# Performance work log

Hardware: AMD Instinct MI355X
Metric: run time of the kernel (lower is better)

Reference implementation:

```python
import jax, jax.numpy as jnp
import numpy as np

DIM = 1024
N_HEADS = 16
HEAD_DIM = DIM // N_HEADS
SCALE = HEAD_DIM ** 0.5


def setup_inputs() -> dict:
    key = jax.random.key(0)
    k_x, k_wqkv, k_bqkv, k_wp, k_bp = jax.random.split(key, 5)
    B, S = 4, 2048
    x = jax.random.normal(k_x, (B, S, DIM), dtype=jnp.float32)
    # Linear params stored input-major: y = x @ W + b
    std_qkv = 1.0 / np.sqrt(DIM)
    W_qkv = jax.random.uniform(k_wqkv, (DIM, 3 * DIM), jnp.float32, -std_qkv, std_qkv)
    b_qkv = jax.random.uniform(k_bqkv, (3 * DIM,), jnp.float32, -std_qkv, std_qkv)
    W_proj = jax.random.uniform(k_wp, (DIM, DIM), jnp.float32, -std_qkv, std_qkv)
    b_proj = jax.random.uniform(k_bp, (DIM,), jnp.float32, -std_qkv, std_qkv)
    return {"x": x, "W_qkv": W_qkv, "b_qkv": b_qkv, "W_proj": W_proj, "b_proj": b_proj}


def reference(x, W_qkv, b_qkv, W_proj, b_proj):
    B, S, D = x.shape
    qkv = x @ W_qkv + b_qkv                       # [B,S,3D]
    Q, K, V = jnp.split(qkv, 3, axis=-1)          # each [B,S,D]
    def heads(t):                                 # [B,S,D] -> [B,H,S,hd]
        return t.reshape(B, S, N_HEADS, HEAD_DIM).transpose(0, 2, 1, 3)
    Q, K, V = heads(Q), heads(K), heads(V)
    scores = jnp.einsum('bhqd,bhkd->bhqk', Q, K) / SCALE   # [B,H,S,S]
    attn = jax.nn.softmax(scores, axis=-1)
    out = jnp.einsum('bhqk,bhkd->bhqd', attn, V)           # [B,H,S,hd]
    out = out.transpose(0, 2, 1, 3).reshape(B, S, D)
    return out @ W_proj + b_proj
```

## Files before the change

### kernel.cpp

```cpp
#include <hip/hip_runtime.h>
#include <hip/hip_bf16.h>

typedef __attribute__((ext_vector_type(8))) __bf16 bf16x8;
typedef __attribute__((ext_vector_type(4))) float f32x4;
typedef __attribute__((ext_vector_type(16))) float f32x16;
typedef __attribute__((ext_vector_type(4))) unsigned int u32x4;

#define DIM 1024
#define NHEADS 16
#define HDIM 64
#define BATCH 4
#define SEQ 2048
#define ROWS (BATCH * SEQ)
#define SCL 0.18033688011112042f

__device__ inline unsigned short f2bf(float f) {
    __hip_bfloat16 h = __float2bfloat16(f);
    return *reinterpret_cast<unsigned short*>(&h);
}

__device__ inline unsigned int packbf2(float a, float b) {
    unsigned short ua = __builtin_bit_cast(unsigned short, (__bf16)a);
    unsigned short ub = __builtin_bit_cast(unsigned short, (__bf16)b);
    return (unsigned int)ua | ((unsigned int)ub << 16);
}

typedef const __attribute__((address_space(1))) unsigned int* gas_ptr;
typedef __attribute__((address_space(3))) unsigned int* las_ptr;
__device__ inline void gload16(const void* g, void* l) {
    __builtin_amdgcn_global_load_lds((gas_ptr)g, (las_ptr)l, 16, 0, 0);
}

__global__ __launch_bounds__(256) void prologue(const float* __restrict__ x,
                                                unsigned short* __restrict__ x_bf,
                                                const float* __restrict__ W_qkv,
                                                unsigned short* __restrict__ WqkvT,
                                                const float* __restrict__ W_proj,
                                                unsigned short* __restrict__ WprojT) {
    __shared__ float tile[32][33];
    const int blk = blockIdx.x;
    if (blk < 8192) {
        int i = blk * 256 + threadIdx.x;
        float4 v = ((const float4*)x)[i];
        ushort4 o;
        o.x = f2bf(v.x); o.y = f2bf(v.y); o.z = f2bf(v.z); o.w = f2bf(v.w);
        ((ushort4*)x_bf)[i] = o;
        return;
    }
    const float* in; unsigned short* outp; int C, srows, bx, byy; float scl;
    if (blk < 11264) {
        int t = blk - 8192;
        in = W_qkv; outp = WqkvT; C = 3 * DIM; srows = DIM; scl = SCL;
        bx = t % 96; byy = t / 96;
    } else {
        int t = blk - 11264;
        in = W_proj; outp = WprojT; C = DIM; srows = 0; scl = 1.f;
        bx = t & 31; byy = t >> 5;
    }
    const int R = DIM;
    int c0 = bx * 32, r0 = byy * 32;
    int tx = threadIdx.x & 31, ty = threadIdx.x >> 5;
#pragma unroll
    for (int i = 0; i < 32; i += 8) {
        int r = r0 + ty + i, c = c0 + tx;
        tile[ty + i][tx] = in[(size_t)r * C + c];
    }
    __syncthreads();
#pragma unroll
    for (int i = 0; i < 32; i += 8) {
        int orow = c0 + ty + i, oc = r0 + tx;
        float v = tile[tx][ty + i];
        if (orow < srows) v *= scl;
        outp[(size_t)orow * R + oc] = f2bf(v);
    }
}

__global__ __launch_bounds__(256) void gemm_bt_bias(const unsigned short* __restrict__ A,
                                                    const unsigned short* __restrict__ Bt,
                                                    const float* __restrict__ bias,
                                                    unsigned short* __restrict__ Cq,
                                                    unsigned short* __restrict__ Kp,
                                                    unsigned short* __restrict__ Vp,
                                                    float* __restrict__ Cf,
                                                    int M, int N, int K, int qcols) {
    __shared__ unsigned short SMEM[18432];
    unsigned short* As0 = SMEM;
    unsigned short* Bs0 = SMEM + 8192;
    const int tid = threadIdx.x;
    const int lane = tid & 63, wave = tid >> 6;
    const int wm = (wave >> 1) * 64, wn = (wave & 1) * 64;
    const int nwg = gridDim.x * gridDim.y;
    const int gflat = blockIdx.y * gridDim.x + blockIdx.x;
    const int bidx = (gflat & 7) * (nwg >> 3) + (gflat >> 3);
    const int bx = bidx % gridDim.x, byy = bidx / gridDim.x;
    const int rowA = byy * 128, rowB = bx * 128;
    const int fr = lane & 15, fo = (lane >> 4) * 8;

    f32x4 acc[4][4] = {};

    for (int k0 = 0; k0 < K; k0 += 64) {
#pragma unroll
        for (int kc = 0; kc < 2; kc++) {
#pragma unroll
            for (int c = 0; c < 2; c++) {
                int o = c * 4096 + tid * 16;
                int r = o >> 6, cb = o & 63;
                int ldsb = c * 4096 + wave * 1024;
                gload16((const char*)A + ((size_t)(rowA + r) * K + k0 + kc * 32) * 2 + cb,
                        (char*)As0 + kc * 8192 + ldsb);
                gload16((const char*)Bt + ((size_t)(rowB + r) * K + k0 + kc * 32) * 2 + cb,
                        (char*)Bs0 + kc * 8192 + ldsb);
            }
        }
        __syncthreads();
#pragma unroll
        for (int kc = 0; kc < 2; kc++) {
            bf16x8 af[4], bfr[4];
#pragma unroll
            for (int i = 0; i < 4; i++) {
                af[i]  = *(const bf16x8*)(As0 + kc * 4096 + (wm + i * 16 + fr) * 32 + fo);
                bfr[i] = *(const bf16x8*)(Bs0 + kc * 4096 + (wn + i * 16 + fr) * 32 + fo);
            }
#pragma unroll
            for (int mi = 0; mi < 4; mi++)
#pragma unroll
                for (int ni = 0; ni < 4; ni++)
                    acc[mi][ni] = __builtin_amdgcn_mfma_f32_16x16x32_bf16(af[mi], bfr[ni],
                                                                          acc[mi][ni], 0, 0, 0);
        }
        __syncthreads();
    }

    const int cn = lane & 15, cm = (lane >> 4) * 4;
    const int gn0 = rowB + wn;

    if (Cf) {
        for (int ni = 0; ni < 4; ni++) {
            int gn = gn0 + ni * 16 + cn;
            float bv = bias[gn];
            if (gn < qcols) bv *= SCL;
            for (int mi = 0; mi < 4; mi++) {
#pragma unroll
                for (int r = 0; r < 4; r++) {
                    int gm = rowA + wm + mi * 16 + cm + r;
                    Cf[(size_t)gm * N + gn] = acc[mi][ni][r] + bv;
                }
            }
        }
    } else if (gn0 < 1024) {
        for (int ni = 0; ni < 4; ni++) {
            int gn = gn0 + ni * 16 + cn;
            float bv = bias[gn];
            if (gn < qcols) bv *= SCL;
            for (int mi = 0; mi < 4; mi++) {
#pragma unroll
                for (int r = 0; r < 4; r++) {
                    int gm = rowA + wm + mi * 16 + cm + r;
                    Cq[(size_t)gm * 1024 + gn] = f2bf(acc[mi][ni][r] + bv);
                }
            }
        }
    } else {
        unsigned short* Lw = SMEM + wave * (64 * 72);
        for (int ni = 0; ni < 4; ni++) {
            float bv = bias[gn0 + ni * 16 + cn];
            for (int mi = 0; mi < 4; mi++) {
#pragma unroll
                for (int r = 0; r < 4; r++)
                    Lw[(mi * 16 + cm + r) * 72 + ni * 16 + cn] = f2bf(acc[mi][ni][r] + bv);
            }
        }
        __builtin_amdgcn_s_waitcnt(0);
        const int b = rowA >> 11, s0g = rowA & 2047;
        const int mm = lane & 31, hh = lane >> 5;
        if (gn0 < 2048) {
            const int h = (gn0 - 1024) >> 6;
            const size_t by = (size_t)(b * 16 + h);
            const int kub = (s0g + wm) >> 5;
#pragma unroll
            for (int f = 0; f < 8; f++) {
                int ktl = f >> 2, ks = f & 3;
                uint4 d = *(const uint4*)&Lw[(ktl * 32 + mm) * 72 + ks * 16 + hh * 8];
                *(uint4*)(Kp + ((by * 64 + kub + ktl) * 4 + ks) * 512 + lane * 8) = d;
            }
        } else {
            const int h = (gn0 - 2048) >> 6;
            const size_t by = (size_t)(b * 16 + h);
            const int vub = (s0g + wm) >> 4;
#pragma unroll
            for (int f = 0; f < 8; f++) {
                int ksl = f >> 1, dt = f & 1;
                unsigned short tmp[8];
#pragma unroll
                for (int j = 0; j < 8; j++)
                    tmp[j] = Lw[(ksl * 16 + (j & 3) + 8 * (j >> 2) + 4 * hh) * 72 + dt * 32 + mm];
                *(uint4*)(Vp + ((by * 128 + vub + ksl) * 2 + dt) * 512 + lane * 8) =
                    *(uint4*)tmp;
            }
        }
    }
}

__device__ inline void softmax_pv(const f32x16& cfrag, const bf16x8 vf[2][2],
                                  f32x16& o0, f32x16& o1, float& psum) {
    unsigned int pk[8];
    float es[8];
#pragma unroll
    for (int p = 0; p < 8; p++) {
        float e0 = __builtin_amdgcn_exp2f(cfrag[2 * p]);
        float e1 = __builtin_amdgcn_exp2f(cfrag[2 * p + 1]);
        es[p] = e0 + e1;
        pk[p] = packbf2(e0, e1);
    }
    psum += ((es[0] + es[1]) + (es[2] + es[3])) + ((es[4] + es[5]) + (es[6] + es[7]));
    u32x4 lo = {pk[0], pk[1], pk[2], pk[3]};
    u32x4 hi = {pk[4], pk[5], pk[6], pk[7]};
    bf16x8 pa0 = __builtin_bit_cast(bf16x8, lo);
    bf16x8 pa1 = __builtin_bit_cast(bf16x8, hi);
    o0 = __builtin_amdgcn_mfma_f32_32x32x16_bf16(pa0, vf[0][0], o0, 0, 0, 0);
    o1 = __builtin_amdgcn_mfma_f32_32x32x16_bf16(pa0, vf[0][1], o1, 0, 0, 0);
    o0 = __builtin_amdgcn_mfma_f32_32x32x16_bf16(pa1, vf[1][0], o0, 0, 0, 0);
    o1 = __builtin_amdgcn_mfma_f32_32x32x16_bf16(pa1, vf[1][1], o1, 0, 0, 0);
}

__device__ inline void attn_step(const bf16x8 kf[4], const bf16x8 vf[2][2],
                                 const bf16x8 qf[2][4], f32x16 oacc[2][2], float psum[2]) {
    f32x16 cf0 = {}, cf1 = {};
#pragma unroll
    for (int ks = 0; ks < 4; ks++)
        cf0 = __builtin_amdgcn_mfma_f32_32x32x16_bf16(kf[ks], qf[0][ks], cf0, 0, 0, 0);
#pragma unroll
    for (int ks = 0; ks < 4; ks++)
        cf1 = __builtin_amdgcn_mfma_f32_32x32x16_bf16(kf[ks], qf[1][ks], cf1, 0, 0, 0);
    softmax_pv(cf0, vf, oacc[0][0], oacc[0][1], psum[0]);
    softmax_pv(cf1, vf, oacc[1][0], oacc[1][1], psum[1]);
}

__global__ __launch_bounds__(256, 2) void attn_kernel(const unsigned short* __restrict__ Qb,
                                                      const unsigned short* __restrict__ Kp,
                                                      const unsigned short* __restrict__ Vp,
                                                      unsigned short* __restrict__ attnb) {
    __shared__ float Po[2][8 * 256];
    __shared__ float Pl[2][128];
    const int tid = threadIdx.x;
    const int lane = tid & 63, wave = tid >> 6;
    const int qpair = wave >> 1, ksplit = wave & 1;
    const int m31 = lane & 31, h = lane >> 5;
    const int gflat = blockIdx.y * gridDim.x + blockIdx.x;
    const int xcd = gflat & 7, slot = gflat >> 3;
    const int by = xcd * 8 + (slot >> 4);
    const int qb = slot & 15;
    const int b = by >> 4;
    const int bS = b * SEQ, hcol = (by & 15) * HDIM;
    const int q0 = qb * 128 + qpair * 64;

    bf16x8 qf[2][4];
#pragma unroll
    for (int qt = 0; qt < 2; qt++)
#pragma unroll
        for (int ks = 0; ks < 4; ks++)
            qf[qt][ks] = *(const bf16x8*)(Qb + (size_t)(bS + q0 + qt * 32 + m31) * 1024 +
                                          hcol + ks * 16 + h * 8);

    f32x16 oacc[2][2] = {};
    float psum[2] = {0.f, 0.f};

    const unsigned short* kbase = Kp + (size_t)by * 64 * 2048 + lane * 8;
    const unsigned short* vbase = Vp + (size_t)by * 128 * 1024 + lane * 8;

    const int ku0 = ksplit * 32;
    bf16x8 kfa[4], kfb[4];
    {
        const unsigned short* kp = kbase + (size_t)ku0 * 2048;
#pragma unroll
        for (int ks = 0; ks < 4; ks++) kfa[ks] = *(const bf16x8*)(kp + ks * 512);
    }
    for (int ki = 0; ki < 32; ki += 2) {
        {
            int ku = ku0 + ki;
            bf16x8 vf[2][2];
#pragma unroll
            for (int ks = 0; ks < 2; ks++) {
                const unsigned short* vp = vbase + ((size_t)ku * 2 + ks) * 1024;
                vf[ks][0] = *(const bf16x8*)(vp);
                vf[ks][1] = *(const bf16x8*)(vp + 512);
            }
            const unsigned short* kpn = kbase + (size_t)(ku + 1) * 2048;
#pragma unroll
            for (int ks = 0; ks < 4; ks++) kfb[ks] = *(const bf16x8*)(kpn + ks * 512);
            attn_step(kfa, vf, qf, oacc, psum);
        }
        {
            int ku = ku0 + ki + 1;
            bf16x8 vf[2][2];
#pragma unroll
            for (int ks = 0; ks < 2; ks++) {
                const unsigned short* vp = vbase + ((size_t)ku * 2 + ks) * 1024;
                vf[ks][0] = *(const bf16x8*)(vp);
                vf[ks][1] = *(const bf16x8*)(vp + 512);
            }
            int kup = ku0 + ((ki + 2 < 32) ? (ki + 2) : 31);
            const unsigned short* kpn = kbase + (size_t)kup * 2048;
#pragma unroll
            for (int ks = 0; ks < 4; ks++) kfa[ks] = *(const bf16x8*)(kpn + ks * 512);
            attn_step(kfb, vf, qf, oacc, psum);
        }
    }

#pragma unroll
    for (int qt = 0; qt < 2; qt++) {
        if (ksplit == 1) {
#pragma unroll
            for (int dt = 0; dt < 2; dt++)
#pragma unroll
                for (int c = 0; c < 4; c++) {
                    f32x4 v = {oacc[qt][dt][c * 4 + 0], oacc[qt][dt][c * 4 + 1],
                               oacc[qt][dt][c * 4 + 2], oacc[qt][dt][c * 4 + 3]};
                    *(f32x4*)&Po[qpair][(dt * 4 + c) * 256 + lane * 4] = v;
                }
            if (qt == 0)
                *(float2*)&Pl[qpair][lane * 2] = make_float2(psum[0], psum[1]);
        }
        __syncthreads();
        if (ksplit == 0) {
#pragma unroll
            for (int dt = 0; dt < 2; dt++)
#pragma unroll
                for (int c = 0; c < 4; c++) {
                    f32x4 v = *(const f32x4*)&Po[qpair][(dt * 4 + c) * 256 + lane * 4];
#pragma unroll
                    for (int j = 0; j < 4; j++) oacc[qt][dt][c * 4 + j] += v[j];
                }
            if (qt == 0) {
                float2 pl = *(const float2*)&Pl[qpair][lane * 2];
                psum[0] += pl.x; psum[1] += pl.y;
            }
        }
        if (qt == 0) __syncthreads();
    }

    if (ksplit == 0) {
#pragma unroll
        for (int qt = 0; qt < 2; qt++) {
            float lt = psum[qt] + __shfl_xor(psum[qt], 32, 64);
            float rl = 1.f / lt;
#pragma unroll
            for (int r = 0; r < 16; r++) {
                int row = (r & 3) + 8 * (r >> 2) + 4 * h;
                float rlr = __shfl(rl, row, 64);
                size_t orow = (size_t)(bS + q0 + qt * 32 + row) * 1024 + hcol;
                attnb[orow + m31]      = f2bf(oacc[qt][0][r] * rlr);
                attnb[orow + 32 + m31] = f2bf(oacc[qt][1][r] * rlr);
            }
        }
    }
}

extern "C" void kernel_launch(void* const* d_in, const int* in_sizes, int n_in,
                              void* d_out, int out_size, void* d_ws, size_t ws_size,
                              hipStream_t stream) {
    const float* x      = (const float*)d_in[0];
    const float* W_qkv  = (const float*)d_in[1];
    const float* b_qkv  = (const float*)d_in[2];
    const float* W_proj = (const float*)d_in[3];
    const float* b_proj = (const float*)d_in[4];
    float* out = (float*)d_out;

    char* ws = (char*)d_ws;
    unsigned short* x_bf   = (unsigned short*)(ws);
    unsigned short* WqkvT  = (unsigned short*)(ws + 16777216);
    unsigned short* Qb     = (unsigned short*)(ws + 23068672);
    unsigned short* Kp     = (unsigned short*)(ws + 39845888);
    unsigned short* Vp     = (unsigned short*)(ws + 56623104);
    unsigned short* WprojT = (unsigned short*)(ws + 73400320);
    unsigned short* attnb  = (unsigned short*)(ws);

    prologue<<<12288, 256, 0, stream>>>(x, x_bf, W_qkv, WqkvT, W_proj, WprojT);

    gemm_bt_bias<<<dim3(3 * DIM / 128, ROWS / 128), 256, 0, stream>>>(
        x_bf, WqkvT, b_qkv, Qb, Kp, Vp, nullptr, ROWS, 3 * DIM, DIM, DIM);

    attn_kernel<<<dim3(SEQ / 128, BATCH * NHEADS), 256, 0, stream>>>(Qb, Kp, Vp, attnb);

    gemm_bt_bias<<<dim3(DIM / 128, ROWS / 128), 256, 0, stream>>>(
        attnb, WprojT, b_proj, nullptr, nullptr, nullptr, out, ROWS, DIM, DIM, 0);
}
```

Measured before the change: 261.8 us.

## Add dedicated 256x256-tile pipelined QKV GEMM with fused K/V packing

Replaces the generic 128x128 GEMM for the QKV projection with a dedicated 512-thread kernel using 256x256 output tiles, 128KB LDS double buffering and direct global-to-LDS loads with XOR swizzle. Loads of the next K-chunk are interleaved between four MFMA phases, and s_setprio is raised around the MFMA blocks. The Q/K/V bias, scale and packing epilogue is moved into the new kernel, and the old GEMM is simplified to the fp32 output projection only. The larger tile raises data reuse and cuts launch count per output, at the cost of lower occupancy and only 384 workgroups.

```diff
diff --git a/kernel.cpp b/kernel.cpp
--- a/kernel.cpp
+++ b/kernel.cpp
@@ -75,15 +75,196 @@
     }
 }
 
+__global__ __launch_bounds__(512, 2) void qkv_gemm_pack(const unsigned short* __restrict__ A,
+                                                        const unsigned short* __restrict__ Bt,
+                                                        const float* __restrict__ bias,
+                                                        unsigned short* __restrict__ Cq,
+                                                        unsigned short* __restrict__ Kp,
+                                                        unsigned short* __restrict__ Vp) {
+    __shared__ __align__(16) char SMEM[131072];
+    const int tid = threadIdx.x;
+    const int lane = tid & 63, wave = tid >> 6;
+    const int wr = wave >> 2, wc = wave & 3;
+    const int fr = lane & 15, lh = lane >> 4;
+    const int gflat = blockIdx.y * gridDim.x + blockIdx.x;
+    const int bidx = (gflat & 7) * 48 + (gflat >> 3);
+    const int bx = bidx % 12, byy = bidx / 12;
+    const int rowA = byy * 256, colB = bx * 256;
+
+    const int sA = wave * 8 + (lane >> 3);
+    const int arow0 = sA;
+    const int crow0 = (sA & 31) + (sA >> 5) * 64;
+    const int glb = ((lane & 7) ^ (lane >> 3)) * 16;
+    const int ga0 = ((lh) ^ (fr & 7)) * 16;
+    const int ga1 = ((4 + lh) ^ (fr & 7)) * 16;
+    const int aoff = (wr * 64 + fr) * 128;
+    const int boff = (wc * 32 + fr) * 128;
+
+    f32x4 acc[8][4] = {};
+
+    auto stA = [&](int tb, int h, int tt) {
+        char* d = SMEM + tb * 65536 + h * 16384 + wave * 1024;
+        const char* g0 = (const char*)A +
+            (((size_t)(rowA + arow0 + h * 64)) * 1024 + (size_t)tt * 64) * 2 + glb;
+        gload16(g0, d);
+        gload16(g0 + (size_t)128 * 2048, d + 8192);
+    };
+    auto stB = [&](int tb, int h, int tt) {
+        char* d = SMEM + tb * 65536 + 32768 + h * 16384 + wave * 1024;
+        const char* g0 = (const char*)Bt +
+            (((size_t)(colB + crow0 + h * 32)) * 1024 + (size_t)tt * 64) * 2 + glb;
+        gload16(g0, d);
+        gload16(g0 + (size_t)128 * 2048, d + 8192);
+    };
+
+    stA(0, 0, 0); stB(0, 0, 0); stA(0, 1, 0); stB(0, 1, 0);
+    stA(1, 0, 1); stB(1, 0, 1);
+    asm volatile("s_waitcnt vmcnt(4)" ::: "memory");
+    __builtin_amdgcn_s_barrier();
+
+    bf16x8 afq[4][2], bfa[2][2], bfb[2][2];
+    for (int u = 0; u < 16; ++u) {
+        const int cur = u & 1;
+        const char* Al = SMEM + cur * 65536;
+        const char* Bl = SMEM + cur * 65536 + 32768;
+#pragma unroll
+        for (int i = 0; i < 4; i++) {
+            afq[i][0] = *(const bf16x8*)(Al + aoff + i * 2048 + ga0);
+            afq[i][1] = *(const bf16x8*)(Al + aoff + i * 2048 + ga1);
+        }
+#pragma unroll
+        for (int j = 0; j < 2; j++) {
+            bfa[j][0] = *(const bf16x8*)(Bl + boff + j * 2048 + ga0);
+            bfa[j][1] = *(const bf16x8*)(Bl + boff + j * 2048 + ga1);
+        }
+        if (u + 1 < 16) stA(cur ^ 1, 1, u + 1);
+        __builtin_amdgcn_s_barrier();
+        __builtin_amdgcn_s_setprio(1);
+#pragma unroll
+        for (int i = 0; i < 4; i++)
+#pragma unroll
+            for (int j = 0; j < 2; j++) {
+                acc[i][j] = __builtin_amdgcn_mfma_f32_16x16x32_bf16(afq[i][0], bfa[j][0], acc[i][j], 0, 0, 0);
+                acc[i][j] = __builtin_amdgcn_mfma_f32_16x16x32_bf16(afq[i][1], bfa[j][1], acc[i][j], 0, 0, 0);
+            }
+        __builtin_amdgcn_s_setprio(0);
+        __builtin_amdgcn_s_barrier();
+#pragma unroll
+        for (int j = 0; j < 2; j++) {
+            bfb[j][0] = *(const bf16x8*)(Bl + 16384 + boff + j * 2048 + ga0);
+            bfb[j][1] = *(const bf16x8*)(Bl + 16384 + boff + j * 2048 + ga1);
+        }
+        if (u + 1 < 16) stB(cur ^ 1, 1, u + 1);
+        __builtin_amdgcn_s_barrier();
+        __builtin_amdgcn_s_setprio(1);
+#pragma unroll
+        for (int i = 0; i < 4; i++)
+#pragma unroll
+            for (int j = 0; j < 2; j++) {
+                acc[i][2 + j] = __builtin_amdgcn_mfma_f32_16x16x32_bf16(afq[i][0], bfb[j][0], acc[i][2 + j], 0, 0, 0);
+                acc[i][2 + j] = __builtin_amdgcn_mfma_f32_16x16x32_bf16(afq[i][1], bfb[j][1], acc[i][2 + j], 0, 0, 0);
+            }
+        __builtin_amdgcn_s_setprio(0);
+        __builtin_amdgcn_s_barrier();
+#pragma unroll
+        for (int i = 0; i < 4; i++) {
+            afq[i][0] = *(const bf16x8*)(Al + 16384 + aoff + i * 2048 + ga0);
+            afq[i][1] = *(const bf16x8*)(Al + 16384 + aoff + i * 2048 + ga1);
+        }
+        if (u + 2 < 16) stA(cur, 0, u + 2);
+        __builtin_amdgcn_s_barrier();
+        __builtin_amdgcn_s_setprio(1);
+#pragma unroll
+        for (int i = 0; i < 4; i++)
+#pragma unroll
+            for (int j = 0; j < 2; j++) {
+                acc[4 + i][j] = __builtin_amdgcn_mfma_f32_16x16x32_bf16(afq[i][0], bfa[j][0], acc[4 + i][j], 0, 0, 0);
+                acc[4 + i][j] = __builtin_amdgcn_mfma_f32_16x16x32_bf16(afq[i][1], bfa[j][1], acc[4 + i][j], 0, 0, 0);
+            }
+        __builtin_amdgcn_s_setprio(0);
+        __builtin_amdgcn_s_barrier();
+        if (u + 2 < 16) stB(cur, 0, u + 2);
+        __builtin_amdgcn_s_barrier();
+        __builtin_amdgcn_s_setprio(1);
+#pragma unroll
+        for (int i = 0; i < 4; i++)
+#pragma unroll
+            for (int j = 0; j < 2; j++) {
+                acc[4 + i][2 + j] = __builtin_amdgcn_mfma_f32_16x16x32_bf16(afq[i][0], bfb[j][0], acc[4 + i][2 + j], 0, 0, 0);
+                acc[4 + i][2 + j] = __builtin_amdgcn_mfma_f32_16x16x32_bf16(afq[i][1], bfb[j][1], acc[4 + i][2 + j], 0, 0, 0);
+            }
+        __builtin_amdgcn_s_setprio(0);
+        if (u < 14) asm volatile("s_waitcnt vmcnt(4)" ::: "memory");
+        else        asm volatile("s_waitcnt vmcnt(0)" ::: "memory");
+        __builtin_amdgcn_s_barrier();
+    }
+
+    const int cm = (lane >> 4) * 4, cn = lane & 15;
+    const int gn0 = colB + wc * 64;
+    if (gn0 < 1024) {
+        for (int ni = 0; ni < 4; ni++) {
+            int gn = gn0 + ni * 16 + cn;
+            float bv = bias[gn] * SCL;
+            for (int mi = 0; mi < 8; mi++) {
+#pragma unroll
+                for (int r = 0; r < 4; r++) {
+                    int gm = rowA + wr * 128 + mi * 16 + cm + r;
+                    Cq[(size_t)gm * 1024 + gn] = f2bf(acc[mi][ni][r] + bv);
+                }
+            }
+        }
+    } else {
+        const int mm = lane & 31, hh = lane >> 5;
+        unsigned short* Lw = (unsigned short*)SMEM + wave * (64 * 72);
+        for (int kg = 0; kg < 2; kg++) {
+            for (int ni = 0; ni < 4; ni++) {
+                float bv = bias[gn0 + ni * 16 + cn];
+                for (int mi = 0; mi < 4; mi++) {
+#pragma unroll
+                    for (int r = 0; r < 4; r++)
+                        Lw[(mi * 16 + cm + r) * 72 + ni * 16 + cn] =
+                            f2bf(acc[kg * 4 + mi][ni][r] + bv);
+                }
+            }
+            __builtin_amdgcn_s_waitcnt(0);
+            const int keybase = rowA + wr * 128 + kg * 64;
+            const int b = keybase >> 11, s0g = keybase & 2047;
+            if (gn0 < 2048) {
+                const int h = (gn0 - 1024) >> 6;
+                const size_t by = (size_t)(b * 16 + h);
+                const int kub = s0g >> 5;
+#pragma unroll
+                for (int f = 0; f < 8; f++) {
+                    int ktl = f >> 2, ks = f & 3;
+                    uint4 d = *(const uint4*)&Lw[(ktl * 32 + mm) * 72 + ks * 16 + hh * 8];
+                    *(uint4*)(Kp + ((by * 64 + kub + ktl) * 4 + ks) * 512 + lane * 8) = d;
+                }
+            } else {
+                const int h = (gn0 - 2048) >> 6;
+                const size_t by = (size_t)(b * 16 + h);
+                const int vub = s0g >> 4;
+#pragma unroll
+                for (int f = 0; f < 8; f++) {
+                    int ksl = f >> 1, dt = f & 1;
+                    unsigned short tmp[8];
+#pragma unroll
+                    for (int j = 0; j < 8; j++)
+                        tmp[j] = Lw[(ksl * 16 + (j & 3) + 8 * (j >> 2) + 4 * hh) * 72 + dt * 32 + mm];
+                    *(uint4*)(Vp + ((by * 128 + vub + ksl) * 2 + dt) * 512 + lane * 8) =
+                        *(uint4*)tmp;
+                }
+            }
+            __builtin_amdgcn_s_waitcnt(0);
+        }
+    }
+}
+
 __global__ __launch_bounds__(256) void gemm_bt_bias(const unsigned short* __restrict__ A,
                                                     const unsigned short* __restrict__ Bt,
                                                     const float* __restrict__ bias,
-                                                    unsigned short* __restrict__ Cq,
-                                                    unsigned short* __restrict__ Kp,
-                                                    unsigned short* __restrict__ Vp,
                                                     float* __restrict__ Cf,
-                                                    int M, int N, int K, int qcols) {
-    __shared__ unsigned short SMEM[18432];
+                                                    int M, int N, int K) {
+    __shared__ unsigned short SMEM[16384];
     unsigned short* As0 = SMEM;
     unsigned short* Bs0 = SMEM + 8192;
     const int tid = threadIdx.x;
@@ -132,70 +313,14 @@
     }
 
     const int cn = lane & 15, cm = (lane >> 4) * 4;
-    const int gn0 = rowB + wn;
-
-    if (Cf) {
-        for (int ni = 0; ni < 4; ni++) {
-            int gn = gn0 + ni * 16 + cn;
-            float bv = bias[gn];
-            if (gn < qcols) bv *= SCL;
-            for (int mi = 0; mi < 4; mi++) {
-#pragma unroll
-                for (int r = 0; r < 4; r++) {
-                    int gm = rowA + wm + mi * 16 + cm + r;
-                    Cf[(size_t)gm * N + gn] = acc[mi][ni][r] + bv;
-                }
-            }
-        }
-    } else if (gn0 < 1024) {
-        for (int ni = 0; ni < 4; ni++) {
-            int gn = gn0 + ni * 16 + cn;
-            float bv = bias[gn];
-            if (gn < qcols) bv *= SCL;
-            for (int mi = 0; mi < 4; mi++) {
-#pragma unroll
-                for (int r = 0; r < 4; r++) {
-                    int gm = rowA + wm + mi * 16 + cm + r;
-                    Cq[(size_t)gm * 1024 + gn] = f2bf(acc[mi][ni][r] + bv);
-                }
-            }
-        }
-    } else {
-        unsigned short* Lw = SMEM + wave * (64 * 72);
-        for (int ni = 0; ni < 4; ni++) {
-            float bv = bias[gn0 + ni * 16 + cn];
-            for (int mi = 0; mi < 4; mi++) {
-#pragma unroll
-                for (int r = 0; r < 4; r++)
-                    Lw[(mi * 16 + cm + r) * 72 + ni * 16 + cn] = f2bf(acc[mi][ni][r] + bv);
-            }
-        }
-        __builtin_amdgcn_s_waitcnt(0);
-        const int b = rowA >> 11, s0g = rowA & 2047;
-        const int mm = lane & 31, hh = lane >> 5;
-        if (gn0 < 2048) {
-            const int h = (gn0 - 1024) >> 6;
-            const size_t by = (size_t)(b * 16 + h);
-            const int kub = (s0g + wm) >> 5;
-#pragma unroll
-            for (int f = 0; f < 8; f++) {
-                int ktl = f >> 2, ks = f & 3;
-                uint4 d = *(const uint4*)&Lw[(ktl * 32 + mm) * 72 + ks * 16 + hh * 8];
-                *(uint4*)(Kp + ((by * 64 + kub + ktl) * 4 + ks) * 512 + lane * 8) = d;
-            }
-        } else {
-            const int h = (gn0 - 2048) >> 6;
-            const size_t by = (size_t)(b * 16 + h);
-            const int vub = (s0g + wm) >> 4;
-#pragma unroll
-            for (int f = 0; f < 8; f++) {
-                int ksl = f >> 1, dt = f & 1;
-                unsigned short tmp[8];
-#pragma unroll
-                for (int j = 0; j < 8; j++)
-                    tmp[j] = Lw[(ksl * 16 + (j & 3) + 8 * (j >> 2) + 4 * hh) * 72 + dt * 32 + mm];
-                *(uint4*)(Vp + ((by * 128 + vub + ksl) * 2 + dt) * 512 + lane * 8) =
-                    *(uint4*)tmp;
+    for (int ni = 0; ni < 4; ni++) {
+        int gn = rowB + wn + ni * 16 + cn;
+        float bv = bias[gn];
+        for (int mi = 0; mi < 4; mi++) {
+#pragma unroll
+            for (int r = 0; r < 4; r++) {
+                int gm = rowA + wm + mi * 16 + cm + r;
+                Cf[(size_t)gm * N + gn] = acc[mi][ni][r] + bv;
             }
         }
     }
@@ -377,11 +502,10 @@
 
     prologue<<<12288, 256, 0, stream>>>(x, x_bf, W_qkv, WqkvT, W_proj, WprojT);
 
-    gemm_bt_bias<<<dim3(3 * DIM / 128, ROWS / 128), 256, 0, stream>>>(
-        x_bf, WqkvT, b_qkv, Qb, Kp, Vp, nullptr, ROWS, 3 * DIM, DIM, DIM);
+    qkv_gemm_pack<<<dim3(12, 32), 512, 0, stream>>>(x_bf, WqkvT, b_qkv, Qb, Kp, Vp);
 
     attn_kernel<<<dim3(SEQ / 128, BATCH * NHEADS), 256, 0, stream>>>(Qb, Kp, Vp, attnb);
 
     gemm_bt_bias<<<dim3(DIM / 128, ROWS / 128), 256, 0, stream>>>(
-        attnb, WprojT, b_proj, nullptr, nullptr, nullptr, out, ROWS, DIM, DIM, 0);
-}
+        attnb, WprojT, b_proj, out, ROWS, DIM, DIM);
+}
```

Result: no change. 261.5 us (-0.1%).
